# Kernel optimization log

Hardware: AMD Instinct MI355X
Metric: run time of the kernel (lower is better)

## Reference

```python
import jax, jax.numpy as jnp
import numpy as np

HID = 50  # HIDDEN_SIZE in source


def _lstm_step(x, h, c, W_ih, W_hh, b):
    # PyTorch LSTM cell: gates order i, f, g, o
    gates = x @ W_ih.T + h @ W_hh.T + b  # [B, 4H]
    i, f, g, o = jnp.split(gates, 4, axis=-1)
    i = jax.nn.sigmoid(i)
    f = jax.nn.sigmoid(f)
    g = jnp.tanh(g)
    o = jax.nn.sigmoid(o)
    c = f * c + i * g
    h = o * jnp.tanh(c)
    return h, c


def setup_inputs() -> dict:
    key = jax.random.key(0)
    ks = jax.random.split(key, 11)
    B, S = 2048, 512
    H, I, O = HID, 1, 1
    s = 1.0 / np.sqrt(H)
    u = lambda k, shp: jax.random.uniform(k, shp, jnp.float32, -s, s)
    return {
        "source": jax.random.normal(ks[0], (B, S, I), jnp.float32),
        "enc_W_ih": u(ks[1], (4 * H, I)),
        "enc_W_hh": u(ks[2], (4 * H, H)),
        "enc_b_ih": u(ks[3], (4 * H,)),
        "enc_b_hh": u(ks[4], (4 * H,)),
        "dec_W_ih": u(ks[5], (4 * H, O)),
        "dec_W_hh": u(ks[6], (4 * H, H)),
        "dec_b_ih": u(ks[7], (4 * H,)),
        "dec_b_hh": u(ks[8], (4 * H,)),
        "fc_W": u(ks[9], (O, H)),
        "fc_b": u(ks[10], (O,)),
        "target_len": 256,
    }


def reference(source, enc_W_ih, enc_W_hh, enc_b_ih, enc_b_hh,
              dec_W_ih, dec_W_hh, dec_b_ih, dec_b_hh, fc_W, fc_b,
              target_len):
    B = source.shape[0]
    H = enc_W_hh.shape[1]
    dt = source.dtype
    h0 = jnp.zeros((B, H), dt)
    c0 = jnp.zeros((B, H), dt)

    enc_b = enc_b_ih + enc_b_hh

    def enc_step(carry, x_t):
        h, c = carry
        h, c = _lstm_step(x_t, h, c, enc_W_ih, enc_W_hh, enc_b)
        return (h, c), None

    # scan over time: [S, B, 1]
    (h, c), _ = jax.lax.scan(enc_step, (h0, c0), jnp.swapaxes(source, 0, 1))

    dec_b = dec_b_ih + dec_b_hh
    x0 = jnp.zeros((B, source.shape[2]), dt)  # decoder_input = zeros

    def dec_step(carry, _):
        x, h, c = carry
        h, c = _lstm_step(x, h, c, dec_W_ih, dec_W_hh, dec_b)
        y = h @ fc_W.T + fc_b  # [B, 1]
        return (y, h, c), y  # feed output back as next input

    _, ys = jax.lax.scan(dec_step, (x0, h, c), None, length=target_len)
    return jnp.swapaxes(ys, 0, 1)  # [B, target_len, 1]
```

## Files before the change

### kernel.cpp

```cpp
#include <hip/hip_runtime.h>


#define HID 50
#define SEQ 512
#define TGT 256
#define MB  4
#define NT  16
#define L2E 1.44269504088896341f

typedef __attribute__((ext_vector_type(8))) _Float16 half8;
typedef __attribute__((ext_vector_type(4))) _Float16 half4;
typedef __attribute__((ext_vector_type(4))) float f32x4;

#define MFMA16(A, B, C) __builtin_amdgcn_mfma_f32_16x16x32_f16((A), (B), (C), 0, 0, 0)

#define GSTEP(XV, IB, OB)                                                   \
    {                                                                       \
        const _Float16* hp_ = &hs[IB][as][ab][0];                           \
        half8 a0 = *(const half8*)(hp_ + kg * 8);           \
        half8 a1 = *(const half8*)(hp_ + 32 + kg * 8);      \
        f32x4 acc[NT];                                                      \
        _Pragma("unroll")                                                   \
        for (int j = 0; j < NT; ++j) {                                      \
            f32x4 z = {0.0f, 0.0f, 0.0f, 0.0f};                             \
            z = MFMA16(a0, Bw[j][0], z);                                    \
            z = MFMA16(a1, Bw[j][1], z);                                    \
            acc[j] = z;                                                     \
        }                                                                   \
        float xv_ = (XV);                                                   \
        float s_[NT], E_[NT], R_[NT];                                       \
        _Pragma("unroll")                                                   \
        for (int j = 0; j < NT; ++j)                                        \
            s_[j] = acc[j][0] + acc[j][2] + fmaf(wx[j], xv_, bb[j]);        \
        _Pragma("unroll")                                                   \
        for (int j = 0; j < NT; ++j)                                        \
            E_[j] = __builtin_amdgcn_exp2f(-s_[j]);                         \
        _Pragma("unroll")                                                   \
        for (int j = 0; j < NT; ++j)                                        \
            R_[j] = __builtin_amdgcn_rcpf(1.0f + E_[j]);                    \
        float e2_[4], r2_[4];                                               \
        _Pragma("unroll")                                                   \
        for (int ug = 0; ug < 4; ++ug) {       \
            float vg = fmaf(2.0f, R_[8 + ug], -1.0f);                       \
            cc[ug] = fmaf(R_[4 + ug], cc[ug], R_[ug] * vg);                 \
            e2_[ug] = __builtin_amdgcn_exp2f(-2.0f * L2E * cc[ug]);         \
        }                                                                   \
        _Pragma("unroll")                                                   \
        for (int ug = 0; ug < 4; ++ug)                                      \
            r2_[ug] = __builtin_amdgcn_rcpf(1.0f + e2_[ug]);                \
        half4 w0_, w1_;                                                     \
        _Pragma("unroll")                                                   \
        for (int ug = 0; ug < 4; ++ug) {                  \
            hv[ug] = R_[12 + ug] * fmaf(2.0f, r2_[ug], -1.0f);              \
            _Float16 q0 = (_Float16)hv[ug];                                 \
            w0_[ug] = q0;                                                   \
            w1_[ug] = (_Float16)(hv[ug] - (float)q0);                       \
        }                                                                   \
        *(half4*)&hs[OB][0][kg][c * 4] = w0_;              \
        *(half4*)&hs[OB][1][kg][c * 4] = w1_;              \
    }

#define DSTEP(T, IB, OB)                                                    \
    {                                                                       \
        GSTEP(xc, IB, OB)                                                   \
        float p = fmaf(fcw0, hv[0],                                         \
                  fmaf(fcw1, hv[1],                                         \
                  fmaf(fcw2, hv[2], fcw3 * hv[3])));                        \
        p += __shfl_xor(p, 1, 64);                                          \
        p += __shfl_xor(p, 2, 64);                                          \
        p += __shfl_xor(p, 4, 64);                                          \
        p += __shfl_xor(p, 8, 64);                                          \
        float y = p + fb;                                                   \
        if (c == 0) ys[kg][T] = y;                                          \
        xc = y;                                                             \
    }

extern "C" __global__ void __launch_bounds__(64, 1)
seq2seq_kernel(const float* __restrict__ src,
               const float* __restrict__ eWih, const float* __restrict__ eWhh,
               const float* __restrict__ eBih, const float* __restrict__ eBhh,
               const float* __restrict__ dWih, const float* __restrict__ dWhh,
               const float* __restrict__ dBih, const float* __restrict__ dBhh,
               const float* __restrict__ fcW, const float* __restrict__ fcB,
               float* __restrict__ out) {
    const int lane = threadIdx.x & 63;
    const int c    = lane & 15;
    const int kg   = lane >> 4;
    const int ab   = c >> 2;
    const int as   = (c >> 1) & 1;
    const int b0   = blockIdx.x * MB;

    __shared__ __align__(16) _Float16 hs[2][2][MB][64];
    __shared__ __align__(16) float srcT[MB][SEQ];
    __shared__ __align__(16) float ys[MB][TGT];

    for (int i = lane; i < 2 * 2 * MB * 64 / 2; i += 64) ((int*)hs)[i] = 0;
    for (int i = lane; i < SEQ * MB; i += 64) {
        int e = i >> 9, t = i & 511;
        srcT[e][t] = src[(size_t)(b0 + e) * SEQ + t];
    }

    half8 Bw[NT][2];
    float wx[NT], bb[NT];
    float cc[4] = {0.0f, 0.0f, 0.0f, 0.0f};
    float hv[4];

    auto loadW = [&](const float* Wih, const float* Whh,
                     const float* Bih, const float* Bhh) {
#pragma unroll
        for (int j = 0; j < NT; ++j) {
            const int g  = j >> 2, ug = j & 3;
            const int u  = ug * 16 + c;
            const bool uv = (u < HID);
            const float sc = (g == 2) ? 2.0f * L2E : L2E;
            const int row = g * HID + (uv ? u : 0);
            wx[j] = uv ? Wih[row] * sc : 0.0f;
            bb[j] = uv ? (Bih[row] + Bhh[row]) * sc : 0.0f;
#pragma unroll
            for (int kt = 0; kt < 2; ++kt) {
                half8 s0;
#pragma unroll
                for (int jj = 0; jj < 8; ++jj) {
                    int kk = kt * 32 + kg * 8 + jj;
                    int us = (kk & 3) * 16 + (kk >> 2);
                    float wv = (uv && us < HID)
                             ? Whh[(size_t)row * HID + us] * sc : 0.0f;
                    s0[jj] = (_Float16)wv;
                }
                Bw[j][kt] = s0;
            }
        }
    };

    loadW(eWih, eWhh, eBih, eBhh);
    for (int t = 0; t < SEQ; t += 2) {
        float2 xp = *(const float2*)&srcT[kg][t];
        { GSTEP(xp.x, 0, 1) }
        { GSTEP(xp.y, 1, 0) }
    }

    loadW(dWih, dWhh, dBih, dBhh);
    const float fcw0 = fcW[c];
    const float fcw1 = fcW[16 + c];
    const float fcw2 = fcW[32 + c];
    const float fcw3 = (48 + c < HID) ? fcW[48 + c] : 0.0f;
    const float fb   = fcB[0];
    float xc = 0.0f;
    for (int t = 0; t < TGT; t += 2) {
        DSTEP(t,     0, 1)
        DSTEP(t + 1, 1, 0)
    }

    for (int i = lane; i < MB * TGT; i += 64) {
        int b = i >> 8, t = i & 255;
        out[(size_t)(b0 + b) * TGT + t] = ys[b][t];
    }
}

extern "C" void kernel_launch(void* const* d_in, const int* in_sizes, int n_in,
                              void* d_out, int out_size, void* d_ws, size_t ws_size,
                              hipStream_t stream) {
    const float* src  = (const float*)d_in[0];
    const float* eWih = (const float*)d_in[1];
    const float* eWhh = (const float*)d_in[2];
    const float* eBih = (const float*)d_in[3];
    const float* eBhh = (const float*)d_in[4];
    const float* dWih = (const float*)d_in[5];
    const float* dWhh = (const float*)d_in[6];
    const float* dBih = (const float*)d_in[7];
    const float* dBhh = (const float*)d_in[8];
    const float* fcW  = (const float*)d_in[9];
    const float* fcB  = (const float*)d_in[10];
    float* out = (float*)d_out;

    const int B = in_sizes[0] / SEQ;
    seq2seq_kernel<<<B / MB, 64, 0, stream>>>(src, eWih, eWhh, eBih, eBhh,
                                              dWih, dWhh, dBih, dBhh,
                                              fcW, fcB, out);
}
```

Before: 564.9 us.

## Halve batch per wave so each lane handles two hidden units

Reduces the batch rows per 64-lane block from four to two and remaps lanes so each lane owns two hidden units instead of four. This halves the per-lane elementwise gate work (exp, rcp, cell update) and doubles the number of blocks, giving more waves to hide the latency of the serial recurrence. The MFMA count per step stays the same, so matrix throughput per batch row halves. The h-state layout, weight permutation and FC reduction (an extra shuffle stage) are reworked to match.

```diff
diff --git a/kernel.cpp b/kernel.cpp
--- a/kernel.cpp
+++ b/kernel.cpp
@@ -4,19 +4,19 @@
 #define HID 50
 #define SEQ 512
 #define TGT 256
-#define MB  4
+#define MB  2
 #define NT  16
 #define L2E 1.44269504088896341f
 
 typedef __attribute__((ext_vector_type(8))) _Float16 half8;
-typedef __attribute__((ext_vector_type(4))) _Float16 half4;
+typedef __attribute__((ext_vector_type(2))) _Float16 half2v;
 typedef __attribute__((ext_vector_type(4))) float f32x4;
 
 #define MFMA16(A, B, C) __builtin_amdgcn_mfma_f32_16x16x32_f16((A), (B), (C), 0, 0, 0)
 
 #define GSTEP(XV, IB, OB)                                                   \
     {                                                                       \
-        const _Float16* hp_ = &hs[IB][as][ab][0];                           \
+        const _Float16* hp_ = &hs[IB][sA][ab][0];                           \
         half8 a0 = *(const half8*)(hp_ + kg * 8);           \
         half8 a1 = *(const half8*)(hp_ + 32 + kg * 8);      \
         f32x4 acc[NT];                                                      \
@@ -28,50 +28,53 @@
             acc[j] = z;                                                     \
         }                                                                   \
         float xv_ = (XV);                                                   \
-        float s_[NT], E_[NT], R_[NT];                                       \
+        float sm[8], E_[8], R_[8];                                          \
         _Pragma("unroll")                                                   \
-        for (int j = 0; j < NT; ++j)                                        \
-            s_[j] = acc[j][0] + acc[j][2] + fmaf(wx[j], xv_, bb[j]);        \
+        for (int g = 0; g < 4; ++g)                                         \
+            _Pragma("unroll")                                               \
+            for (int l = 0; l < 2; ++l) {                                   \
+                int j = g * 4 + ugp2 + l, i = g * 2 + l;                    \
+                sm[i] = acc[j][0] + acc[j][1] + fmaf(wx[i], xv_, bb[i]);    \
+            }                                                               \
         _Pragma("unroll")                                                   \
-        for (int j = 0; j < NT; ++j)                                        \
-            E_[j] = __builtin_amdgcn_exp2f(-s_[j]);                         \
+        for (int i = 0; i < 8; ++i)                                         \
+            E_[i] = __builtin_amdgcn_exp2f(-sm[i]);                         \
         _Pragma("unroll")                                                   \
-        for (int j = 0; j < NT; ++j)                                        \
-            R_[j] = __builtin_amdgcn_rcpf(1.0f + E_[j]);                    \
-        float e2_[4], r2_[4];                                               \
+        for (int i = 0; i < 8; ++i)                                         \
+            R_[i] = __builtin_amdgcn_rcpf(1.0f + E_[i]);                    \
+        float e2_[2], r2_[2];                                               \
         _Pragma("unroll")                                                   \
-        for (int ug = 0; ug < 4; ++ug) {       \
-            float vg = fmaf(2.0f, R_[8 + ug], -1.0f);                       \
-            cc[ug] = fmaf(R_[4 + ug], cc[ug], R_[ug] * vg);                 \
-            e2_[ug] = __builtin_amdgcn_exp2f(-2.0f * L2E * cc[ug]);         \
+        for (int l = 0; l < 2; ++l) {       \
+            float vg = fmaf(2.0f, R_[4 + l], -1.0f);                        \
+            cc[l] = fmaf(R_[2 + l], cc[l], R_[l] * vg);                     \
+            e2_[l] = __builtin_amdgcn_exp2f(-2.0f * L2E * cc[l]);           \
         }                                                                   \
         _Pragma("unroll")                                                   \
-        for (int ug = 0; ug < 4; ++ug)                                      \
-            r2_[ug] = __builtin_amdgcn_rcpf(1.0f + e2_[ug]);                \
-        half4 w0_, w1_;                                                     \
+        for (int l = 0; l < 2; ++l)                                         \
+            r2_[l] = __builtin_amdgcn_rcpf(1.0f + e2_[l]);                  \
+        half2v w0_, w1_;                                                    \
         _Pragma("unroll")                                                   \
-        for (int ug = 0; ug < 4; ++ug) {                  \
-            hv[ug] = R_[12 + ug] * fmaf(2.0f, r2_[ug], -1.0f);              \
-            _Float16 q0 = (_Float16)hv[ug];                                 \
-            w0_[ug] = q0;                                                   \
-            w1_[ug] = (_Float16)(hv[ug] - (float)q0);                       \
+        for (int l = 0; l < 2; ++l) {                       \
+            hv[l] = R_[6 + l] * fmaf(2.0f, r2_[l], -1.0f);                  \
+            _Float16 q0 = (_Float16)hv[l];                                  \
+            w0_[l] = q0;                                                    \
+            w1_[l] = (_Float16)(hv[l] - (float)q0);                         \
         }                                                                   \
-        *(half4*)&hs[OB][0][kg][c * 4] = w0_;              \
-        *(half4*)&hs[OB][1][kg][c * 4] = w1_;              \
+        *(half2v*)&hs[OB][0][kgb][p0] = w0_;               \
+        *(half2v*)&hs[OB][1][kgb][p0] = w1_;               \
     }
 
 #define DSTEP(T, IB, OB)                                                    \
     {                                                                       \
         GSTEP(xc, IB, OB)                                                   \
-        float p = fmaf(fcw0, hv[0],                                         \
-                  fmaf(fcw1, hv[1],                                         \
-                  fmaf(fcw2, hv[2], fcw3 * hv[3])));                        \
+        float p = fmaf(fcw0, hv[0], fcw1 * hv[1]);                          \
         p += __shfl_xor(p, 1, 64);                                          \
         p += __shfl_xor(p, 2, 64);                                          \
         p += __shfl_xor(p, 4, 64);                                          \
         p += __shfl_xor(p, 8, 64);                                          \
+        p += __shfl_xor(p, 16, 64);                                         \
         float y = p + fb;                                                   \
-        if (c == 0) ys[kg][T] = y;                                          \
+        if ((lane & 31) == 0) ys[kgb][T] = y;                               \
         xc = y;                                                             \
     }
 
@@ -86,24 +89,28 @@
     const int lane = threadIdx.x & 63;
     const int c    = lane & 15;
     const int kg   = lane >> 4;
-    const int ab   = c >> 2;
-    const int as   = (c >> 1) & 1;
+    const int kgb  = kg >> 1;
+    const int ugp  = kg & 1;
+    const int ugp2 = 2 * ugp;
+    const int ab   = c >> 3;
+    const int sA   = c & 1;
     const int b0   = blockIdx.x * MB;
+    const int p0   = 32 * ugp + 2 * c;
 
-    __shared__ __align__(16) _Float16 hs[2][2][MB][64];
+    __shared__ __align__(16) _Float16 hs[2][2][MB][72];
     __shared__ __align__(16) float srcT[MB][SEQ];
     __shared__ __align__(16) float ys[MB][TGT];
 
-    for (int i = lane; i < 2 * 2 * MB * 64 / 2; i += 64) ((int*)hs)[i] = 0;
+    for (int i = lane; i < 2 * 2 * MB * 72 / 2; i += 64) ((int*)hs)[i] = 0;
     for (int i = lane; i < SEQ * MB; i += 64) {
         int e = i >> 9, t = i & 511;
         srcT[e][t] = src[(size_t)(b0 + e) * SEQ + t];
     }
 
     half8 Bw[NT][2];
-    float wx[NT], bb[NT];
-    float cc[4] = {0.0f, 0.0f, 0.0f, 0.0f};
-    float hv[4];
+    float wx[8], bb[8];
+    float cc[2] = {0.0f, 0.0f};
+    float hv[2];
 
     auto loadW = [&](const float* Wih, const float* Whh,
                      const float* Bih, const float* Bhh) {
@@ -114,15 +121,14 @@
             const bool uv = (u < HID);
             const float sc = (g == 2) ? 2.0f * L2E : L2E;
             const int row = g * HID + (uv ? u : 0);
-            wx[j] = uv ? Wih[row] * sc : 0.0f;
-            bb[j] = uv ? (Bih[row] + Bhh[row]) * sc : 0.0f;
 #pragma unroll
             for (int kt = 0; kt < 2; ++kt) {
                 half8 s0;
 #pragma unroll
                 for (int jj = 0; jj < 8; ++jj) {
-                    int kk = kt * 32 + kg * 8 + jj;
-                    int us = (kk & 3) * 16 + (kk >> 2);
+                    int p = kt * 32 + kg * 8 + jj;
+                    int d = p >> 1, e = p & 1;
+                    int us = 32 * (d >> 4) + (d & 15) + 16 * e;
                     float wv = (uv && us < HID)
                              ? Whh[(size_t)row * HID + us] * sc : 0.0f;
                     s0[jj] = (_Float16)wv;
@@ -130,20 +136,31 @@
                 Bw[j][kt] = s0;
             }
         }
+#pragma unroll
+        for (int g = 0; g < 4; ++g)
+#pragma unroll
+            for (int l = 0; l < 2; ++l) {
+                const int u = (ugp2 + l) * 16 + c;
+                const bool uv = (u < HID);
+                const float sc = (g == 2) ? 2.0f * L2E : L2E;
+                const int row = g * HID + (uv ? u : 0);
+                wx[g * 2 + l] = uv ? Wih[row] * sc : 0.0f;
+                bb[g * 2 + l] = uv ? (Bih[row] + Bhh[row]) * sc : 0.0f;
+            }
     };
 
     loadW(eWih, eWhh, eBih, eBhh);
     for (int t = 0; t < SEQ; t += 2) {
-        float2 xp = *(const float2*)&srcT[kg][t];
+        float2 xp = *(const float2*)&srcT[kgb][t];
         { GSTEP(xp.x, 0, 1) }
         { GSTEP(xp.y, 1, 0) }
     }
 
     loadW(dWih, dWhh, dBih, dBhh);
-    const float fcw0 = fcW[c];
-    const float fcw1 = fcW[16 + c];
-    const float fcw2 = fcW[32 + c];
-    const float fcw3 = (48 + c < HID) ? fcW[48 + c] : 0.0f;
+    const int u0f = 32 * ugp + c;
+    const int u1f = u0f + 16;
+    const float fcw0 = fcW[u0f];
+    const float fcw1 = (u1f < HID) ? fcW[u1f] : 0.0f;
     const float fb   = fcB[0];
     float xc = 0.0f;
     for (int t = 0; t < TGT; t += 2) {
```

Result: slower. 2.157 ms (+281.8%).

## Map one batch element per wave with one hidden unit per lane

Applied to the files above, without the earlier changes.

Restructures the LSTM so each 64-lane wave handles a single batch element, with each lane owning one hidden unit, instead of four batch elements per wave with four units per lane. The MFMA computes a 16-row tile but only one row is useful, so most matrix work is wasted in exchange for far less per-lane transcendental and elementwise work. Blocks now hold two waves, one sleeping briefly at the start to stagger them, and decoder outputs go straight to global memory from lane 0 instead of being staged in shared memory. The grid grows from 512 to 1024 blocks, which raises parallelism while adding redundant MFMA work per batch element.

```diff
diff --git a/kernel.cpp b/kernel.cpp
--- a/kernel.cpp
+++ b/kernel.cpp
@@ -4,78 +4,70 @@
 #define HID 50
 #define SEQ 512
 #define TGT 256
-#define MB  4
-#define NT  16
 #define L2E 1.44269504088896341f
 
 typedef __attribute__((ext_vector_type(8))) _Float16 half8;
-typedef __attribute__((ext_vector_type(4))) _Float16 half4;
 typedef __attribute__((ext_vector_type(4))) float f32x4;
 
 #define MFMA16(A, B, C) __builtin_amdgcn_mfma_f32_16x16x32_f16((A), (B), (C), 0, 0, 0)
 
 #define GSTEP(XV, IB, OB)                                                   \
     {                                                                       \
-        const _Float16* hp_ = &hs[IB][as][ab][0];                           \
-        half8 a0 = *(const half8*)(hp_ + kg * 8);           \
-        half8 a1 = *(const half8*)(hp_ + 32 + kg * 8);      \
-        f32x4 acc[NT];                                                      \
+        const _Float16* hp_ = &hs[w][IB][sA][0];                            \
+        half8 a0 = *(const half8*)(hp_ + kg * 8);             \
+        half8 a1 = *(const half8*)(hp_ + 32 + kg * 8);        \
+        f32x4 acc[16];                                                      \
         _Pragma("unroll")                                                   \
-        for (int j = 0; j < NT; ++j) {                                      \
+        for (int j = 0; j < 16; ++j) {                                      \
             f32x4 z = {0.0f, 0.0f, 0.0f, 0.0f};                             \
             z = MFMA16(a0, Bw[j][0], z);                                    \
             z = MFMA16(a1, Bw[j][1], z);                                    \
             acc[j] = z;                                                     \
         }                                                                   \
+        float sums[16];                                                     \
+        _Pragma("unroll")                                                   \
+        for (int j = 0; j < 16; ++j)                                        \
+            sums[j] = acc[j][0] + acc[j][1];           \
         float xv_ = (XV);                                                   \
-        float s_[NT], E_[NT], R_[NT];                                       \
+        float sm[4], R_[4];                                                 \
         _Pragma("unroll")                                                   \
-        for (int j = 0; j < NT; ++j)                                        \
-            s_[j] = acc[j][0] + acc[j][2] + fmaf(wx[j], xv_, bb[j]);        \
-        _Pragma("unroll")                                                   \
-        for (int j = 0; j < NT; ++j)                                        \
-            E_[j] = __builtin_amdgcn_exp2f(-s_[j]);                         \
-        _Pragma("unroll")                                                   \
-        for (int j = 0; j < NT; ++j)                                        \
-            R_[j] = __builtin_amdgcn_rcpf(1.0f + E_[j]);                    \
-        float e2_[4], r2_[4];                                               \
-        _Pragma("unroll")                                                   \
-        for (int ug = 0; ug < 4; ++ug) {       \
-            float vg = fmaf(2.0f, R_[8 + ug], -1.0f);                       \
-            cc[ug] = fmaf(R_[4 + ug], cc[ug], R_[ug] * vg);                 \
-            e2_[ug] = __builtin_amdgcn_exp2f(-2.0f * L2E * cc[ug]);         \
+        for (int g = 0; g < 4; ++g) {                   \
+            float s01 = (kg & 1) ? sums[g * 4 + 1] : sums[g * 4 + 0];       \
+            float s23 = (kg & 1) ? sums[g * 4 + 3] : sums[g * 4 + 2];       \
+            float sg  = (kg & 2) ? s23 : s01;                               \
+            sm[g] = sg + fmaf(wx[g], xv_, bb[g]);                           \
         }                                                                   \
         _Pragma("unroll")                                                   \
-        for (int ug = 0; ug < 4; ++ug)                                      \
-            r2_[ug] = __builtin_amdgcn_rcpf(1.0f + e2_[ug]);                \
-        half4 w0_, w1_;                                                     \
-        _Pragma("unroll")                                                   \
-        for (int ug = 0; ug < 4; ++ug) {                  \
-            hv[ug] = R_[12 + ug] * fmaf(2.0f, r2_[ug], -1.0f);              \
-            _Float16 q0 = (_Float16)hv[ug];                                 \
-            w0_[ug] = q0;                                                   \
-            w1_[ug] = (_Float16)(hv[ug] - (float)q0);                       \
-        }                                                                   \
-        *(half4*)&hs[OB][0][kg][c * 4] = w0_;              \
-        *(half4*)&hs[OB][1][kg][c * 4] = w1_;              \
+        for (int g = 0; g < 4; ++g)                                         \
+            R_[g] = __builtin_amdgcn_rcpf(1.0f +                            \
+                        __builtin_amdgcn_exp2f(-sm[g]));                    \
+        float vg = fmaf(2.0f, R_[2], -1.0f);             \
+        cc = fmaf(R_[1], cc, R_[0] * vg);                                   \
+        float r2 = __builtin_amdgcn_rcpf(1.0f +                             \
+                       __builtin_amdgcn_exp2f(-2.0f * L2E * cc));           \
+        hv = R_[3] * fmaf(2.0f, r2, -1.0f);                                 \
+        _Float16 q0 = (_Float16)hv;                                         \
+        _Float16 q1 = (_Float16)(hv - (float)q0);                           \
+        hs[w][OB][0][u] = q0;                                   \
+        hs[w][OB][1][u] = q1;                                   \
     }
 
 #define DSTEP(T, IB, OB)                                                    \
     {                                                                       \
         GSTEP(xc, IB, OB)                                                   \
-        float p = fmaf(fcw0, hv[0],                                         \
-                  fmaf(fcw1, hv[1],                                         \
-                  fmaf(fcw2, hv[2], fcw3 * hv[3])));                        \
+        float p = fcw * hv;                                                 \
         p += __shfl_xor(p, 1, 64);                                          \
         p += __shfl_xor(p, 2, 64);                                          \
         p += __shfl_xor(p, 4, 64);                                          \
         p += __shfl_xor(p, 8, 64);                                          \
+        p += __shfl_xor(p, 16, 64);                                         \
+        p += __shfl_xor(p, 32, 64);                                         \
         float y = p + fb;                                                   \
-        if (c == 0) ys[kg][T] = y;                                          \
+        if (lane == 0) out[(size_t)b * TGT + (T)] = y;                      \
         xc = y;                                                             \
     }
 
-extern "C" __global__ void __launch_bounds__(64, 1)
+extern "C" __global__ void __launch_bounds__(128, 2)
 seq2seq_kernel(const float* __restrict__ src,
                const float* __restrict__ eWih, const float* __restrict__ eWhh,
                const float* __restrict__ eBih, const float* __restrict__ eBhh,
@@ -83,77 +75,73 @@
                const float* __restrict__ dBih, const float* __restrict__ dBhh,
                const float* __restrict__ fcW, const float* __restrict__ fcB,
                float* __restrict__ out) {
-    const int lane = threadIdx.x & 63;
+    const int tid  = threadIdx.x;
+    const int w    = tid >> 6;
+    const int lane = tid & 63;
     const int c    = lane & 15;
     const int kg   = lane >> 4;
-    const int ab   = c >> 2;
-    const int as   = (c >> 1) & 1;
-    const int b0   = blockIdx.x * MB;
+    const int sA   = c & 1;
+    const int u    = kg * 16 + c;
+    const int b    = blockIdx.x * 2 + w;
 
-    __shared__ __align__(16) _Float16 hs[2][2][MB][64];
-    __shared__ __align__(16) float srcT[MB][SEQ];
-    __shared__ __align__(16) float ys[MB][TGT];
+    __shared__ __align__(16) _Float16 hs[2][2][2][64];
+    __shared__ __align__(16) float srcT[2][SEQ];
 
-    for (int i = lane; i < 2 * 2 * MB * 64 / 2; i += 64) ((int*)hs)[i] = 0;
-    for (int i = lane; i < SEQ * MB; i += 64) {
-        int e = i >> 9, t = i & 511;
-        srcT[e][t] = src[(size_t)(b0 + e) * SEQ + t];
-    }
+    for (int i = lane; i < 2 * 2 * 64 / 2; i += 64) ((int*)&hs[w])[i] = 0;
+    for (int i = lane; i < SEQ; i += 64)
+        srcT[w][i] = src[(size_t)b * SEQ + i];
 
-    half8 Bw[NT][2];
-    float wx[NT], bb[NT];
-    float cc[4] = {0.0f, 0.0f, 0.0f, 0.0f};
-    float hv[4];
+    half8 Bw[16][2];
+    float wx[4], bb[4];
+    float cc = 0.0f, hv;
 
     auto loadW = [&](const float* Wih, const float* Whh,
                      const float* Bih, const float* Bhh) {
 #pragma unroll
-        for (int j = 0; j < NT; ++j) {
+        for (int j = 0; j < 16; ++j) {
             const int g  = j >> 2, ug = j & 3;
-            const int u  = ug * 16 + c;
-            const bool uv = (u < HID);
+            const int uo = ug * 16 + c;
+            const bool uv = (uo < HID);
             const float sc = (g == 2) ? 2.0f * L2E : L2E;
-            const int row = g * HID + (uv ? u : 0);
-            wx[j] = uv ? Wih[row] * sc : 0.0f;
-            bb[j] = uv ? (Bih[row] + Bhh[row]) * sc : 0.0f;
+            const int row = g * HID + (uv ? uo : 0);
 #pragma unroll
             for (int kt = 0; kt < 2; ++kt) {
                 half8 s0;
 #pragma unroll
                 for (int jj = 0; jj < 8; ++jj) {
-                    int kk = kt * 32 + kg * 8 + jj;
-                    int us = (kk & 3) * 16 + (kk >> 2);
-                    float wv = (uv && us < HID)
-                             ? Whh[(size_t)row * HID + us] * sc : 0.0f;
+                    int k = kt * 32 + kg * 8 + jj;
+                    float wv = (uv && k < HID)
+                             ? Whh[(size_t)row * HID + k] * sc : 0.0f;
                     s0[jj] = (_Float16)wv;
                 }
                 Bw[j][kt] = s0;
             }
         }
+#pragma unroll
+        for (int g = 0; g < 4; ++g) {
+            const bool uv = (u < HID);
+            const float sc = (g == 2) ? 2.0f * L2E : L2E;
+            const int row = g * HID + (uv ? u : 0);
+            wx[g] = uv ? Wih[row] * sc : 0.0f;
+            bb[g] = uv ? (Bih[row] + Bhh[row]) * sc : 0.0f;
+        }
     };
 
     loadW(eWih, eWhh, eBih, eBhh);
+    if (w == 1) __builtin_amdgcn_s_sleep(7);
     for (int t = 0; t < SEQ; t += 2) {
-        float2 xp = *(const float2*)&srcT[kg][t];
+        float2 xp = *(const float2*)&srcT[w][t];
         { GSTEP(xp.x, 0, 1) }
         { GSTEP(xp.y, 1, 0) }
     }
 
     loadW(dWih, dWhh, dBih, dBhh);
-    const float fcw0 = fcW[c];
-    const float fcw1 = fcW[16 + c];
-    const float fcw2 = fcW[32 + c];
-    const float fcw3 = (48 + c < HID) ? fcW[48 + c] : 0.0f;
-    const float fb   = fcB[0];
+    const float fcw = (u < HID) ? fcW[u] : 0.0f;
+    const float fb  = fcB[0];
     float xc = 0.0f;
     for (int t = 0; t < TGT; t += 2) {
         DSTEP(t,     0, 1)
         DSTEP(t + 1, 1, 0)
-    }
-
-    for (int i = lane; i < MB * TGT; i += 64) {
-        int b = i >> 8, t = i & 255;
-        out[(size_t)(b0 + b) * TGT + t] = ys[b][t];
     }
 }
 
@@ -174,7 +162,7 @@
     float* out = (float*)d_out;
 
     const int B = in_sizes[0] / SEQ;
-    seq2seq_kernel<<<B / MB, 64, 0, stream>>>(src, eWih, eWhh, eBih, eBhh,
+    seq2seq_kernel<<<B / 2, 128, 0, stream>>>(src, eWih, eWhh, eBih, eBhh,
                                               dWih, dWhh, dBih, dBhh,
                                               fcW, fcB, out);
 }
```

Result: slower. 883.0 us (+56.3%).
